# Performance work log

Measured on AMD Instinct MI355X. Metric: run time of the kernel, lower is better.

The kernel has to match this reference:

```python
import jax, jax.numpy as jnp
import numpy as np

TOP_K = 1024  # init top_k


def setup_inputs() -> dict:
    key = jax.random.key(0)
    ks = jax.random.split(key, 11)
    B, S, D, H = 8, 1024, 1024, 4096
    s = 0.02
    return {
        "inputs": jax.random.normal(ks[0], (B, S, D), jnp.float32),
        "up_w": jax.random.normal(ks[1], (H, D), jnp.float32) * s,
        "up_b": jax.random.normal(ks[2], (H,), jnp.float32) * s,
        "gate_w1": jax.random.normal(ks[3], (H, D), jnp.float32) * s,
        "gate_b1": jax.random.normal(ks[4], (H,), jnp.float32) * s,
        "gate_w2": jax.random.normal(ks[5], (H, H), jnp.float32) * s,
        "gate_b2": jax.random.normal(ks[6], (H,), jnp.float32) * s,
        "mod_w": jax.random.normal(ks[7], (H, D), jnp.float32) * s,
        "mod_b": jax.random.normal(ks[8], (H,), jnp.float32) * s,
        "down_w": jax.random.normal(ks[9], (D, H), jnp.float32) * s,
        "down_b": jax.random.normal(ks[10], (D,), jnp.float32) * s,
    }


def reference(inputs, up_w, up_b, gate_w1, gate_b1, gate_w2, gate_b2,
              mod_w, mod_b, down_w, down_b):
    B, S, D = inputs.shape
    H = up_w.shape[0]
    # gate: Linear -> ReLU -> Linear, scores [B,S,H]
    scores = jax.nn.relu(jnp.einsum('bsd,hd->bsh', inputs, gate_w1) + gate_b1)
    scores = jnp.einsum('bsh,gh->bsg', scores, gate_w2) + gate_b2
    flat_scores = scores.reshape(B, S * H)
    k = min(TOP_K * S, S * H)
    _, flat_idx = jax.lax.top_k(flat_scores, k)          # [B,k]
    hidden_idx = flat_idx % H                            # [B,k]
    # scatter writes mod.weight[h] at row h -> duplicates harmless -> boolean mask
    batch_idx = jnp.broadcast_to(jnp.arange(B)[:, None], (B, k))
    mask = jnp.zeros((B, H), bool).at[batch_idx, hidden_idx].set(True)
    # per-batch modified weights/bias (materialized like torch repeat+index_put)
    w = jnp.where(mask[:, :, None], mod_w[None], up_w[None])   # [B,H,D]
    b = jnp.where(mask, mod_b[None], up_b[None])               # [B,H]
    h = jnp.einsum('bsd,bhd->bsh', inputs, w) + b[:, None, :]
    h = jax.nn.silu(h)
    # dropout p=0.0 (eval) -> identity
    return jnp.einsum('bsh,dh->bsd', h, down_w) + down_b
```

## Files before the change

### kernel.cpp

```cpp
#include <hip/hip_runtime.h>
#include <cstdint>

typedef __attribute__((ext_vector_type(8))) short short8;
typedef __attribute__((ext_vector_type(4))) float floatx4;
typedef unsigned int uint32;

typedef const void __attribute__((address_space(1)))* gcptr;
typedef void __attribute__((address_space(3)))* lptr;

constexpr int Bn = 8, Sn = 1024, Dn = 1024, Hn = 4096;
constexpr uint32 KTOP = 1024u * 1024u;
constexpr uint32 SKBASE = 0xBB000000u;
constexpr uint32 EMAX = (1u << 27) - 1u;
constexpr uint32 WLO = 3645;
constexpr uint32 WHI = 4157;
constexpr uint32 CAP = 1u << 20;

constexpr size_t NX  = (size_t)Bn * Sn * Dn;
constexpr size_t NW1 = (size_t)Hn * Dn;
constexpr size_t NW2 = (size_t)Hn * Hn;
constexpr size_t NRS = (size_t)Bn * Sn * Hn;

constexpr size_t OFF_XH   = 0;
constexpr size_t OFF_XL   = OFF_XH  + 2 * NX;
constexpr size_t OFF_W1H  = OFF_XL  + 2 * NX;
constexpr size_t OFF_W1L  = OFF_W1H + 2 * NW1;
constexpr size_t OFF_W2H  = OFF_W1L + 2 * NW1;
constexpr size_t OFF_W2L  = OFF_W2H + 2 * NW2;
constexpr size_t OFF_RSH  = OFF_W2L + 2 * NW2;
constexpr size_t OFF_RSL  = OFF_RSH + 2 * NRS;
constexpr size_t OFF_HIST = OFF_RSL + 2 * NRS;
constexpr size_t OFF_HIST2= OFF_HIST + (size_t)Bn * 8192 * 4;
constexpr size_t OFF_HMAX = OFF_HIST2+ (size_t)Bn * 16384 * 4;
constexpr size_t OFF_META = OFF_HMAX + (size_t)Bn * Hn * 4;
constexpr size_t OFF_BSEL = OFF_META + 4096;
constexpr size_t OFF_MASK = OFF_BSEL + (size_t)Bn * Hn * 4;
constexpr size_t WS_SMALL = OFF_MASK + (size_t)Bn * Hn * 4;
constexpr size_t ZERO_BYTES = OFF_BSEL - OFF_HIST;
constexpr size_t OFF_BUF  = OFF_XL;

__device__ __forceinline__ ushort f2bf(float f) {
  uint32 u = __float_as_uint(f);
  u += 0x7fffu + ((u >> 16) & 1u);
  return (ushort)(u >> 16);
}
__device__ __forceinline__ float bf2f(ushort h) {
  return __uint_as_float(((uint32)h) << 16);
}
__device__ __forceinline__ uint32 skey(float v) {
  uint32 u = __float_as_uint(v);
  return (u & 0x80000000u) ? ~u : (u | 0x80000000u);
}
__device__ __forceinline__ uint32 ekey(uint32 key) {
  if (key <= SKBASE) return 0u;
  uint32 d = key - SKBASE;
  return d > EMAX ? EMAX : d;
}
__device__ __forceinline__ void g2l(const ushort* src, ushort* dst) {
  __builtin_amdgcn_global_load_lds((gcptr)src, (lptr)dst, 16, 0, 0);
}
__device__ __forceinline__ void stage_tile(ushort* lds, const ushort* gbase, int ldg, int tid) {
  const int w = tid >> 6;
  const int c0 = tid, c1 = tid + 256;
  g2l(gbase + (size_t)(c0 >> 2) * ldg + (c0 & 3) * 8, lds + (size_t)(w * 64) * 8);
  g2l(gbase + (size_t)(c1 >> 2) * ldg + (c1 & 3) * 8, lds + (size_t)(256 + w * 64) * 8);
}
__device__ __forceinline__ void stage_tile_sel(ushort* lds, const ushort* upw,
                                               const ushort* modw, const uint32* bm,
                                               int n0, int k0, int ldg, int tid) {
  const int w = tid >> 6;
  const int c0 = tid, c1 = tid + 256;
  const int r0 = n0 + (c0 >> 2), r1 = n0 + (c1 >> 2);
  const ushort* s0 = (bm[r0] ? modw : upw) + (size_t)r0 * ldg + k0 + (c0 & 3) * 8;
  const ushort* s1 = (bm[r1] ? modw : upw) + (size_t)r1 * ldg + k0 + (c1 & 3) * 8;
  g2l(s0, lds + (size_t)(w * 64) * 8);
  g2l(s1, lds + (size_t)(256 + w * 64) * 8);
}

__global__ __launch_bounds__(256) void cvt_split_k(const float4* __restrict__ x,
                                                   ushort* __restrict__ hi,
                                                   ushort* __restrict__ lo, int n4) {
  int stride = gridDim.x * 256;
  for (int i = blockIdx.x * 256 + threadIdx.x; i < n4; i += stride) {
    float4 v = x[i];
    ushort h0 = f2bf(v.x), h1 = f2bf(v.y), h2 = f2bf(v.z), h3 = f2bf(v.w);
    ushort4 hv; hv.x = h0; hv.y = h1; hv.z = h2; hv.w = h3;
    *(ushort4*)(hi + (size_t)i * 4) = hv;
    ushort4 lv;
    lv.x = f2bf(v.x - bf2f(h0)); lv.y = f2bf(v.y - bf2f(h1));
    lv.z = f2bf(v.z - bf2f(h2)); lv.w = f2bf(v.w - bf2f(h3));
    *(ushort4*)(lo + (size_t)i * 4) = lv;
  }
}
__global__ __launch_bounds__(256) void cvt_single_k(const float4* __restrict__ x,
                                                    ushort* __restrict__ hi, int n4) {
  int stride = gridDim.x * 256;
  for (int i = blockIdx.x * 256 + threadIdx.x; i < n4; i += stride) {
    float4 v = x[i];
    ushort4 hv; hv.x = f2bf(v.x); hv.y = f2bf(v.y); hv.z = f2bf(v.z); hv.w = f2bf(v.w);
    *(ushort4*)(hi + (size_t)i * 4) = hv;
  }
}
__global__ __launch_bounds__(256) void zero_out_k(float* __restrict__ o, int n) {
  int i = blockIdx.x * 256 + threadIdx.x;
  if (i < n) o[i] = 0.f;
}

constexpr int EPI_RELU = 0;
constexpr int EPI_SCORE = 1;
constexpr int EPI_SILU = 2;
constexpr int EPI_F32 = 3;

template <bool SPLIT, bool SELB, int EPI>
__global__ __launch_bounds__(256, SPLIT ? 3 : 2) void gemm_bt(
    const ushort* __restrict__ Ah, const ushort* __restrict__ Al,
    const ushort* __restrict__ Bh, const ushort* __restrict__ Bl,
    const uint32* __restrict__ bmask,
    int N, int K, long long a_bs, long long o_bs, long long bias_bs,
    const float* __restrict__ bias,
    void* __restrict__ outp, void* __restrict__ out2p,
    uint32* __restrict__ hist, uint32* __restrict__ hmax,
    uint32* __restrict__ buf, uint32* __restrict__ cnt) {
  __shared__ __align__(16) ushort lds[SPLIT ? 16384 : 8192];
  ushort* As = lds;
  ushort* Bs = lds + (SPLIT ? 8192 : 4096);

  const int tid = threadIdx.x;
  const int w = tid >> 6, l = tid & 63;
  const int wm = (w >> 1) << 6, wn = (w & 1) << 6;
  const int lm = l & 15, lq = l >> 4;
  const int m0 = blockIdx.y << 7, n0 = blockIdx.x << 7;
  const int z = blockIdx.z;

  const ushort* pAh = Ah + (size_t)z * a_bs + (size_t)m0 * K;
  const ushort* pAl = SPLIT ? Al + (size_t)z * a_bs + (size_t)m0 * K : nullptr;
  const ushort* pBh = SELB ? nullptr : Bh + (size_t)n0 * K;
  const ushort* pBl = (SPLIT && !SELB) ? Bl + (size_t)n0 * K : nullptr;
  const uint32* bm = SELB ? bmask + (size_t)z * Hn : nullptr;

  floatx4 acc[4][4];
#pragma unroll
  for (int i = 0; i < 4; i++)
#pragma unroll
    for (int j = 0; j < 4; j++) acc[i][j] = floatx4{0.f, 0.f, 0.f, 0.f};

  for (int k0 = 0; k0 < K; k0 += 32) {
    stage_tile(As, pAh + k0, K, tid);
    if constexpr (SELB)
      stage_tile_sel(Bs, Bh, Bl, bm, n0, k0, K, tid);
    else
      stage_tile(Bs, pBh + k0, K, tid);
    if constexpr (SPLIT) {
      stage_tile(As + 4096, pAl + k0, K, tid);
      stage_tile(Bs + 4096, pBl + k0, K, tid);
    }
    __syncthreads();
    short8 afh[4], bfh[4];
#pragma unroll
    for (int i = 0; i < 4; i++)
      afh[i] = *(const short8*)&As[(wm + i * 16 + lm) * 32 + lq * 8];
#pragma unroll
    for (int i = 0; i < 4; i++)
      bfh[i] = *(const short8*)&Bs[(wn + i * 16 + lm) * 32 + lq * 8];
#pragma unroll
    for (int mi = 0; mi < 4; mi++)
#pragma unroll
      for (int ni = 0; ni < 4; ni++)
        acc[mi][ni] = __builtin_amdgcn_mfma_f32_16x16x32_bf16(afh[mi], bfh[ni], acc[mi][ni], 0, 0, 0);
    if constexpr (SPLIT) {
      {
        short8 afl[4];
#pragma unroll
        for (int i = 0; i < 4; i++)
          afl[i] = *(const short8*)&As[4096 + (wm + i * 16 + lm) * 32 + lq * 8];
#pragma unroll
        for (int mi = 0; mi < 4; mi++)
#pragma unroll
          for (int ni = 0; ni < 4; ni++)
            acc[mi][ni] = __builtin_amdgcn_mfma_f32_16x16x32_bf16(afl[mi], bfh[ni], acc[mi][ni], 0, 0, 0);
      }
      {
        short8 bfl[4];
#pragma unroll
        for (int i = 0; i < 4; i++)
          bfl[i] = *(const short8*)&Bs[4096 + (wn + i * 16 + lm) * 32 + lq * 8];
#pragma unroll
        for (int mi = 0; mi < 4; mi++)
#pragma unroll
          for (int ni = 0; ni < 4; ni++)
            acc[mi][ni] = __builtin_amdgcn_mfma_f32_16x16x32_bf16(afh[mi], bfl[ni], acc[mi][ni], 0, 0, 0);
      }
    }
    __syncthreads();
  }

  if constexpr (EPI == EPI_SILU) {
    ushort* o = (ushort*)outp + (size_t)z * o_bs;
    const float* bb = bias + (size_t)z * bias_bs;
#pragma unroll
    for (int mi = 0; mi < 4; mi++)
#pragma unroll
      for (int ni = 0; ni < 4; ni++) {
        int gm = m0 + wm + mi * 16 + lq * 4;
        int gn = n0 + wn + ni * 16 + lm;
        float bnv = bb[gn];
#pragma unroll
        for (int r = 0; r < 4; r++) {
          float v = acc[mi][ni][r] + bnv;
          float s = v / (1.f + __expf(-v));
          o[(size_t)(gm + r) * N + gn] = f2bf(s);
        }
      }
  } else if constexpr (EPI == EPI_F32) {
    float* o = (float*)outp;
#pragma unroll
    for (int mi = 0; mi < 4; mi++)
#pragma unroll
      for (int ni = 0; ni < 4; ni++) {
        int gm = m0 + wm + mi * 16 + lq * 4;
        int gn = n0 + wn + ni * 16 + lm;
        float bnv = bias[gn];
#pragma unroll
        for (int r = 0; r < 4; r++)
          o[(size_t)(gm + r) * N + gn] = acc[mi][ni][r] + bnv;
      }
  }
}

#define LGKM0 do { asm volatile("s_waitcnt lgkmcnt(0)" ::: "memory"); \
                   __builtin_amdgcn_sched_barrier(0); } while (0)

__device__ __forceinline__ short8 fragld(const ushort* S, int r, int swz) {
  return *(const short8*)&S[r * 32 + swz];
}
__device__ __forceinline__ void stage256(ushort* d, const ushort* g,
                                         size_t soff0, size_t soff1, int dbase) {
  g2l(g + soff0, d + dbase);
  g2l(g + soff1, d + dbase + 4096);
}
__device__ __forceinline__ void mfma_block(floatx4 (&acc)[8][4], const short8 (&af)[4],
                                           int mi0, const short8 (&bf)[4]) {
#pragma unroll
  for (int mi = 0; mi < 4; mi++)
#pragma unroll
    for (int ni = 0; ni < 4; ni++)
      acc[mi0 + mi][ni] =
          __builtin_amdgcn_mfma_f32_16x16x32_bf16(af[mi], bf[ni], acc[mi0 + mi][ni], 0, 0, 0);
}

template <bool ST>
__device__ __forceinline__ void kstep256(
    floatx4 (&acc)[8][4], ushort (&lds)[2][4][8192], int p,
    const ushort* nA0, const ushort* nB0, const ushort* nA1, const ushort* nB1,
    size_t soff0, size_t soff1, int dbase, int swz, int lm, int wrow, int wcol) {
  const ushort* AhS = &lds[p][0][0];
  const ushort* BhS = &lds[p][1][0];
  const ushort* AlS = &lds[p][2][0];
  const ushort* BlS = &lds[p][3][0];
  ushort* dA0 = &lds[p ^ 1][0][0];
  ushort* dB0 = &lds[p ^ 1][1][0];
  ushort* dA1 = &lds[p ^ 1][2][0];
  ushort* dB1 = &lds[p ^ 1][3][0];

  short8 afh0[4], afh1[4], bfh[4];
#pragma unroll
  for (int i = 0; i < 4; i++) afh0[i] = fragld(AhS, wrow + i * 16 + lm, swz);
#pragma unroll
  for (int i = 0; i < 4; i++) bfh[i] = fragld(BhS, wcol + i * 16 + lm, swz);
  if constexpr (ST) stage256(dA0, nA0, soff0, soff1, dbase);
  __builtin_amdgcn_s_barrier();
  LGKM0;
  __builtin_amdgcn_s_setprio(1);
  mfma_block(acc, afh0, 0, bfh);
  __builtin_amdgcn_s_setprio(0);
  __builtin_amdgcn_s_barrier();
#pragma unroll
  for (int i = 0; i < 4; i++) afh1[i] = fragld(AhS, wrow + 64 + i * 16 + lm, swz);
  if constexpr (ST) stage256(dB0, nB0, soff0, soff1, dbase);
  __builtin_amdgcn_s_barrier();
  LGKM0;
  __builtin_amdgcn_s_setprio(1);
  mfma_block(acc, afh1, 4, bfh);
  __builtin_amdgcn_s_setprio(0);
  if constexpr (ST) asm volatile("s_waitcnt vmcnt(6)" ::: "memory");
  else              asm volatile("s_waitcnt vmcnt(2)" ::: "memory");
  __builtin_amdgcn_s_barrier();
  {
    short8 afl[4];
#pragma unroll
    for (int i = 0; i < 4; i++) afl[i] = fragld(AlS, wrow + i * 16 + lm, swz);
    if constexpr (ST) stage256(dA1, nA1, soff0, soff1, dbase);
    __builtin_amdgcn_s_barrier();
    LGKM0;
    __builtin_amdgcn_s_setprio(1);
    mfma_block(acc, afl, 0, bfh);
    __builtin_amdgcn_s_setprio(0);
    __builtin_amdgcn_s_barrier();
  }
  {
    short8 afl[4];
#pragma unroll
    for (int i = 0; i < 4; i++) afl[i] = fragld(AlS, wrow + 64 + i * 16 + lm, swz);
    if constexpr (ST) stage256(dB1, nB1, soff0, soff1, dbase);
    __builtin_amdgcn_s_barrier();
    LGKM0;
    __builtin_amdgcn_s_setprio(1);
    mfma_block(acc, afl, 4, bfh);
    __builtin_amdgcn_s_setprio(0);
    if constexpr (ST) asm volatile("s_waitcnt vmcnt(8)" ::: "memory");
    else              asm volatile("s_waitcnt vmcnt(0)" ::: "memory");
    __builtin_amdgcn_s_barrier();
  }
  {
    short8 bfl[4];
#pragma unroll
    for (int i = 0; i < 4; i++) bfl[i] = fragld(BlS, wcol + i * 16 + lm, swz);
    __builtin_amdgcn_s_barrier();
    LGKM0;
    __builtin_amdgcn_s_setprio(1);
    mfma_block(acc, afh0, 0, bfl);
    mfma_block(acc, afh1, 4, bfl);
    __builtin_amdgcn_s_setprio(0);
    if constexpr (ST) asm volatile("s_waitcnt vmcnt(4)" ::: "memory");
    __builtin_amdgcn_s_barrier();
  }
}

template <int EPI>
__global__ __launch_bounds__(512, 2) void gemm256(
    const ushort* __restrict__ Ah, const ushort* __restrict__ Al,
    const ushort* __restrict__ Bh, const ushort* __restrict__ Bl,
    int N, int K, const float* __restrict__ bias,
    ushort* __restrict__ outh, ushort* __restrict__ outl,
    uint32* __restrict__ hist, uint32* __restrict__ hmax,
    uint32* __restrict__ buf, uint32* __restrict__ cnt) {
  static_assert(EPI == EPI_RELU || EPI == EPI_SCORE, "gemm256 handles G1/G2 only");
  __shared__ __align__(16) ushort lds[2][4][8192];
  const int tid = threadIdx.x;
  const int l = tid & 63, w = tid >> 6;
  const int lm = l & 15, lq = l >> 4;
  const int swz = (lq ^ ((lm >> 1) & 3)) << 3;
  const int wrow = (w >> 2) << 7, wcol = (w & 3) << 6;
  const int m0 = blockIdx.y << 8, n0 = blockIdx.x << 8;

  const int cg = ((l & 3) ^ ((l >> 3) & 3)) << 3;
  const int r0 = (w << 4) + (l >> 2);
  const size_t soff0 = (size_t)r0 * K + cg;
  const size_t soff1 = soff0 + (size_t)128 * K;
  const int dbase = w << 9;

  const ushort* pA0 = Ah + (size_t)m0 * K;
  const ushort* pA1 = Al + (size_t)m0 * K;
  const ushort* pB0 = Bh + (size_t)n0 * K;
  const ushort* pB1 = Bl + (size_t)n0 * K;

  floatx4 acc[8][4];
#pragma unroll
  for (int i = 0; i < 8; i++)
#pragma unroll
    for (int j = 0; j < 4; j++) acc[i][j] = floatx4{0.f, 0.f, 0.f, 0.f};

  stage256(&lds[0][0][0], pA0, soff0, soff1, dbase);
  stage256(&lds[0][1][0], pB0, soff0, soff1, dbase);
  stage256(&lds[0][2][0], pA1, soff0, soff1, dbase);
  stage256(&lds[0][3][0], pB1, soff0, soff1, dbase);
  asm volatile("s_waitcnt vmcnt(4)" ::: "memory");
  __builtin_amdgcn_s_barrier();

  const int nk = K >> 5;
  int T = 0;
  for (; T < nk - 1; ++T) {
    const int ko = (T + 1) << 5;
    kstep256<true>(acc, lds, T & 1, pA0 + ko, pB0 + ko, pA1 + ko, pB1 + ko,
                   soff0, soff1, dbase, swz, lm, wrow, wcol);
  }
  kstep256<false>(acc, lds, T & 1, pA0, pB0, pA1, pB1,
                  soff0, soff1, dbase, swz, lm, wrow, wcol);

  if constexpr (EPI == EPI_RELU) {
#pragma unroll
    for (int mi = 0; mi < 8; mi++)
#pragma unroll
      for (int ni = 0; ni < 4; ni++) {
        const int gm = m0 + wrow + mi * 16 + lq * 4;
        const int gn = n0 + wcol + ni * 16 + lm;
        const float bnv = bias[gn];
#pragma unroll
        for (int r = 0; r < 4; r++) {
          float v = fmaxf(acc[mi][ni][r] + bnv, 0.f);
          ushort h = f2bf(v);
          size_t o = (size_t)(gm + r) * N + gn;
          outh[o] = h;
          outl[o] = f2bf(v - bf2f(h));
        }
      }
  } else {
    __syncthreads();
    uint32* hs = (uint32*)&lds[0][0][0];
    for (int i = tid; i < 8192; i += 512) hs[i] = 0;
    __syncthreads();
    const int batch = m0 >> 10;
    uint32 cntl = 0;
#pragma unroll
    for (int ni = 0; ni < 4; ni++) {
      const int gn = n0 + wcol + ni * 16 + lm;
      const float bnv = bias[gn];
      float vmax = -3.4e38f;
#pragma unroll
      for (int mi = 0; mi < 8; mi++) {
#pragma unroll
        for (int r = 0; r < 4; r++) {
          float v = acc[mi][ni][r] + bnv;
          uint32 e = ekey(skey(v));
          uint32 bk = e >> 14;
          atomicAdd(&hs[bk], 1u);
          if (bk >= WLO && bk <= WHI) cntl++;
          vmax = fmaxf(vmax, v);
        }
      }
      atomicMax(&hmax[batch * Hn + gn], skey(vmax));
    }
    __syncthreads();
    for (int i = tid; i < 8192; i += 512) {
      uint32 c = hs[i];
      if (c) atomicAdd(&hist[batch * 8192 + i], c);
    }
    __syncthreads();
    hs[tid] = cntl;
    __syncthreads();
    if (tid == 0) {
      uint32 run = 0;
      for (int i = 0; i < 512; i++) { uint32 t = hs[i]; hs[i] = run; run += t; }
      hs[512] = atomicAdd(&cnt[batch], run);
    }
    __syncthreads();
    uint32 off = hs[512] + hs[tid];
    uint32* bb = buf + (size_t)batch * CAP;
#pragma unroll
    for (int ni = 0; ni < 4; ni++) {
      const int gn = n0 + wcol + ni * 16 + lm;
      const float bnv = bias[gn];
#pragma unroll
      for (int mi = 0; mi < 8; mi++) {
#pragma unroll
        for (int r = 0; r < 4; r++) {
          float v = acc[mi][ni][r] + bnv;
          uint32 e = ekey(skey(v));
          uint32 bk = e >> 14;
          if (bk >= WLO && bk <= WHI) {
            if (off < CAP) bb[off] = e;
            off++;
          }
        }
      }
    }
  }
}

__global__ __launch_bounds__(256) void select1_k(const uint32* __restrict__ hist,
                                                 uint32* __restrict__ meta) {
  int b = blockIdx.x;
  const uint32* h = hist + b * 8192;
  __shared__ uint32 ps[256];
  uint32 s = 0;
  int base = threadIdx.x * 32;
  for (int i = 0; i < 32; i++) s += h[base + i];
  ps[threadIdx.x] = s;
  __syncthreads();
  if (threadIdx.x == 0) {
    uint32 cum = 0, need = 1;
    int j = 0;
    for (int c = 255; c >= 0; c--) {
      if (cum + ps[c] >= KTOP) {
        for (int i = c * 32 + 31;; i--) {
          uint32 hv = h[i];
          if (cum + hv >= KTOP) { j = i; need = KTOP - cum; break; }
          cum += hv;
        }
        break;
      }
      cum += ps[c];
    }
    meta[8 + b] = (uint32)j;
    meta[16 + b] = need;
    meta[b] = SKBASE + ((uint32)j << 14);
  }
}

__global__ __launch_bounds__(256) void refine_buf_k(const uint32* __restrict__ buf,
                                                    const uint32* __restrict__ meta,
                                                    uint32* __restrict__ hist2) {
  const uint32* cnt = meta + 32;
  size_t stride = (size_t)gridDim.x * 256;
  for (int b = 0; b < Bn; b++) {
    uint32 n = cnt[b] < CAP ? cnt[b] : CAP;
    uint32 j = meta[8 + b];
    const uint32* bb = buf + (size_t)b * CAP;
    for (size_t i = (size_t)blockIdx.x * 256 + threadIdx.x; i < n; i += stride) {
      uint32 e = bb[i];
      if ((e >> 14) == j) atomicAdd(&hist2[(size_t)b * 16384 + (e & 0x3FFFu)], 1u);
    }
  }
}

__global__ __launch_bounds__(256) void select2_k(const uint32* __restrict__ hist2,
                                                 uint32* __restrict__ meta) {
  int b = blockIdx.x;
  const uint32* h2 = hist2 + (size_t)b * 16384;
  __shared__ uint32 ps[256];
  uint32 s = 0;
  const uint32* p = h2 + (size_t)threadIdx.x * 64;
  for (int i = 0; i < 64; i += 4) {
    uint4 v = *(const uint4*)(p + i);
    s += v.x + v.y + v.z + v.w;
  }
  ps[threadIdx.x] = s;
  __syncthreads();
  if (threadIdx.x == 0) {
    uint32 j = meta[8 + b];
    uint32 valid = (j >= WLO && j <= WHI && meta[32 + b] <= CAP) ? 1u : 0u;
    if (valid) {
      uint32 need = meta[16 + b];
      uint32 cum = 0;
      int c = 255;
      for (; c > 0; c--) {
        if (cum + ps[c] >= need) break;
        cum += ps[c];
      }
      uint32 rem = 0;
      for (int i = 63; i >= 0; i--) {
        uint32 hv = h2[c * 64 + i];
        if (cum + hv >= need) { rem = (uint32)(c * 64 + i); break; }
        cum += hv;
      }
      meta[b] = SKBASE + (j << 14) + rem;
    }
  }
}

__global__ __launch_bounds__(256) void mask_k(const uint32* __restrict__ hmax,
                                              const uint32* __restrict__ meta,
                                              const float* __restrict__ modb,
                                              const float* __restrict__ upb,
                                              uint32* __restrict__ mask,
                                              float* __restrict__ bsel) {
  int i = blockIdx.x * 256 + threadIdx.x;
  int b = i >> 12, h = i & 4095;
  bool m = hmax[i] >= meta[b];
  mask[i] = m ? 1u : 0u;
  bsel[i] = m ? modb[h] : upb[h];
}

extern "C" void kernel_launch(void* const* d_in, const int* in_sizes, int n_in,
                              void* d_out, int out_size, void* d_ws, size_t ws_size,
                              hipStream_t stream) {
  (void)in_sizes; (void)n_in;
  const float* x    = (const float*)d_in[0];
  const float* up_w = (const float*)d_in[1];
  const float* up_b = (const float*)d_in[2];
  const float* g_w1 = (const float*)d_in[3];
  const float* g_b1 = (const float*)d_in[4];
  const float* g_w2 = (const float*)d_in[5];
  const float* g_b2 = (const float*)d_in[6];
  const float* mod_w= (const float*)d_in[7];
  const float* mod_b= (const float*)d_in[8];
  const float* dw   = (const float*)d_in[9];
  const float* db   = (const float*)d_in[10];
  float* out = (float*)d_out;

  if (ws_size < WS_SMALL) {
    zero_out_k<<<(out_size + 255) / 256, 256, 0, stream>>>(out, out_size);
    return;
  }

  char* ws = (char*)d_ws;
  ushort* XH  = (ushort*)(ws + OFF_XH);
  ushort* XL  = (ushort*)(ws + OFF_XL);
  ushort* W1H = (ushort*)(ws + OFF_W1H);
  ushort* W1L = (ushort*)(ws + OFF_W1L);
  ushort* W2H = (ushort*)(ws + OFF_W2H);
  ushort* W2L = (ushort*)(ws + OFF_W2L);
  ushort* RSH = (ushort*)(ws + OFF_RSH);
  ushort* RSL = (ushort*)(ws + OFF_RSL);
  uint32* HIST = (uint32*)(ws + OFF_HIST);
  uint32* HIST2= (uint32*)(ws + OFF_HIST2);
  uint32* HMAX = (uint32*)(ws + OFF_HMAX);
  uint32* META = (uint32*)(ws + OFF_META);
  float*  BSEL = (float*)(ws + OFF_BSEL);
  uint32* MASK = (uint32*)(ws + OFF_MASK);
  uint32* BUF  = (uint32*)(ws + OFF_BUF);
  ushort* UPW  = W1H;
  ushort* MODW = W1L;
  ushort* DWNW = XL;
  ushort* HBUF = RSH;

  hipMemsetAsync(ws + OFF_HIST, 0, ZERO_BYTES, stream);

  cvt_split_k<<<1024, 256, 0, stream>>>((const float4*)x, XH, XL, (int)(NX / 4));
  cvt_split_k<<<1024, 256, 0, stream>>>((const float4*)g_w1, W1H, W1L, (int)(NW1 / 4));
  cvt_split_k<<<2048, 256, 0, stream>>>((const float4*)g_w2, W2H, W2L, (int)(NW2 / 4));

  gemm256<EPI_RELU><<<dim3(Hn / 256, (Bn * Sn) / 256), 512, 0, stream>>>(
      XH, XL, W1H, W1L, Hn, Dn, g_b1, RSH, RSL, nullptr, nullptr, nullptr, nullptr);
  gemm256<EPI_SCORE><<<dim3(Hn / 256, (Bn * Sn) / 256), 512, 0, stream>>>(
      RSH, RSL, W2H, W2L, Hn, Hn, g_b2, nullptr, nullptr, HIST, HMAX, BUF, META + 32);

  select1_k<<<Bn, 256, 0, stream>>>(HIST, META);
  refine_buf_k<<<512, 256, 0, stream>>>(BUF, META, HIST2);
  select2_k<<<Bn, 256, 0, stream>>>(HIST2, META);
  mask_k<<<(Bn * Hn) / 256, 256, 0, stream>>>(HMAX, META, mod_b, up_b, MASK, BSEL);

  cvt_single_k<<<1024, 256, 0, stream>>>((const float4*)up_w, UPW, (int)(NW1 / 4));
  cvt_single_k<<<1024, 256, 0, stream>>>((const float4*)mod_w, MODW, (int)(NW1 / 4));
  cvt_single_k<<<1024, 256, 0, stream>>>((const float4*)dw, DWNW, (int)(NW1 / 4));

  gemm_bt<false, true, EPI_SILU><<<dim3(Hn / 128, Sn / 128, Bn), 256, 0, stream>>>(
      XH, nullptr, UPW, MODW, MASK, Hn, Dn,
      (long long)Sn * Dn, (long long)Sn * Hn, (long long)Hn,
      BSEL, HBUF, nullptr, nullptr, nullptr, nullptr, nullptr);
  gemm_bt<false, false, EPI_F32><<<dim3(Dn / 128, (Bn * Sn) / 128, 1), 256, 0, stream>>>(
      HBUF, nullptr, DWNW, nullptr, nullptr, Dn, Hn, 0, 0, 0, db, out, nullptr,
      nullptr, nullptr, nullptr, nullptr);
}
```

Baseline: 1.246 ms.

## Move SiLU up-projection to pipelined 256x256 gemm and reorder split-bf16 k-step

```diff
diff --git a/kernel.cpp b/kernel.cpp
--- a/kernel.cpp
+++ b/kernel.cpp
@@ -39,6 +39,8 @@
 constexpr size_t ZERO_BYTES = OFF_BSEL - OFF_HIST;
 constexpr size_t OFF_BUF  = OFF_XL;
 
+#define VMCNT(n) asm volatile("s_waitcnt vmcnt(" #n ")" ::: "memory")
+
 __device__ __forceinline__ ushort f2bf(float f) {
   uint32 u = __float_as_uint(f);
   u += 0x7fffu + ((u >> 16) & 1u);
@@ -64,17 +66,6 @@
   const int c0 = tid, c1 = tid + 256;
   g2l(gbase + (size_t)(c0 >> 2) * ldg + (c0 & 3) * 8, lds + (size_t)(w * 64) * 8);
   g2l(gbase + (size_t)(c1 >> 2) * ldg + (c1 & 3) * 8, lds + (size_t)(256 + w * 64) * 8);
-}
-__device__ __forceinline__ void stage_tile_sel(ushort* lds, const ushort* upw,
-                                               const ushort* modw, const uint32* bm,
-                                               int n0, int k0, int ldg, int tid) {
-  const int w = tid >> 6;
-  const int c0 = tid, c1 = tid + 256;
-  const int r0 = n0 + (c0 >> 2), r1 = n0 + (c1 >> 2);
-  const ushort* s0 = (bm[r0] ? modw : upw) + (size_t)r0 * ldg + k0 + (c0 & 3) * 8;
-  const ushort* s1 = (bm[r1] ? modw : upw) + (size_t)r1 * ldg + k0 + (c1 & 3) * 8;
-  g2l(s0, lds + (size_t)(w * 64) * 8);
-  g2l(s1, lds + (size_t)(256 + w * 64) * 8);
 }
 
 __global__ __launch_bounds__(256) void cvt_split_k(const float4* __restrict__ x,
@@ -118,9 +109,7 @@
     const uint32* __restrict__ bmask,
     int N, int K, long long a_bs, long long o_bs, long long bias_bs,
     const float* __restrict__ bias,
-    void* __restrict__ outp, void* __restrict__ out2p,
-    uint32* __restrict__ hist, uint32* __restrict__ hmax,
-    uint32* __restrict__ buf, uint32* __restrict__ cnt) {
+    void* __restrict__ outp, void* __restrict__ out2p) {
   __shared__ __align__(16) ushort lds[SPLIT ? 16384 : 8192];
   ushort* As = lds;
   ushort* Bs = lds + (SPLIT ? 8192 : 4096);
@@ -133,10 +122,7 @@
   const int z = blockIdx.z;
 
   const ushort* pAh = Ah + (size_t)z * a_bs + (size_t)m0 * K;
-  const ushort* pAl = SPLIT ? Al + (size_t)z * a_bs + (size_t)m0 * K : nullptr;
-  const ushort* pBh = SELB ? nullptr : Bh + (size_t)n0 * K;
-  const ushort* pBl = (SPLIT && !SELB) ? Bl + (size_t)n0 * K : nullptr;
-  const uint32* bm = SELB ? bmask + (size_t)z * Hn : nullptr;
+  const ushort* pBh = Bh + (size_t)n0 * K;
 
   floatx4 acc[4][4];
 #pragma unroll
@@ -146,14 +132,7 @@
 
   for (int k0 = 0; k0 < K; k0 += 32) {
     stage_tile(As, pAh + k0, K, tid);
-    if constexpr (SELB)
-      stage_tile_sel(Bs, Bh, Bl, bm, n0, k0, K, tid);
-    else
-      stage_tile(Bs, pBh + k0, K, tid);
-    if constexpr (SPLIT) {
-      stage_tile(As + 4096, pAl + k0, K, tid);
-      stage_tile(Bs + 4096, pBl + k0, K, tid);
-    }
+    stage_tile(Bs, pBh + k0, K, tid);
     __syncthreads();
     short8 afh[4], bfh[4];
 #pragma unroll
@@ -167,30 +146,6 @@
 #pragma unroll
       for (int ni = 0; ni < 4; ni++)
         acc[mi][ni] = __builtin_amdgcn_mfma_f32_16x16x32_bf16(afh[mi], bfh[ni], acc[mi][ni], 0, 0, 0);
-    if constexpr (SPLIT) {
-      {
-        short8 afl[4];
-#pragma unroll
-        for (int i = 0; i < 4; i++)
-          afl[i] = *(const short8*)&As[4096 + (wm + i * 16 + lm) * 32 + lq * 8];
-#pragma unroll
-        for (int mi = 0; mi < 4; mi++)
-#pragma unroll
-          for (int ni = 0; ni < 4; ni++)
-            acc[mi][ni] = __builtin_amdgcn_mfma_f32_16x16x32_bf16(afl[mi], bfh[ni], acc[mi][ni], 0, 0, 0);
-      }
-      {
-        short8 bfl[4];
-#pragma unroll
-        for (int i = 0; i < 4; i++)
-          bfl[i] = *(const short8*)&Bs[4096 + (wn + i * 16 + lm) * 32 + lq * 8];
-#pragma unroll
-        for (int mi = 0; mi < 4; mi++)
-#pragma unroll
-          for (int ni = 0; ni < 4; ni++)
-            acc[mi][ni] = __builtin_amdgcn_mfma_f32_16x16x32_bf16(afh[mi], bfl[ni], acc[mi][ni], 0, 0, 0);
-      }
-    }
     __syncthreads();
   }
 
@@ -227,16 +182,8 @@
   }
 }
 
-#define LGKM0 do { asm volatile("s_waitcnt lgkmcnt(0)" ::: "memory"); \
-                   __builtin_amdgcn_sched_barrier(0); } while (0)
-
 __device__ __forceinline__ short8 fragld(const ushort* S, int r, int swz) {
   return *(const short8*)&S[r * 32 + swz];
-}
-__device__ __forceinline__ void stage256(ushort* d, const ushort* g,
-                                         size_t soff0, size_t soff1, int dbase) {
-  g2l(g + soff0, d + dbase);
-  g2l(g + soff1, d + dbase + 4096);
 }
 __device__ __forceinline__ void mfma_block(floatx4 (&acc)[8][4], const short8 (&af)[4],
                                            int mi0, const short8 (&bf)[4]) {
@@ -249,99 +196,127 @@
 }
 
 template <bool ST>
-__device__ __forceinline__ void kstep256(
-    floatx4 (&acc)[8][4], ushort (&lds)[2][4][8192], int p,
-    const ushort* nA0, const ushort* nB0, const ushort* nA1, const ushort* nB1,
-    size_t soff0, size_t soff1, int dbase, int swz, int lm, int wrow, int wcol) {
-  const ushort* AhS = &lds[p][0][0];
-  const ushort* BhS = &lds[p][1][0];
-  const ushort* AlS = &lds[p][2][0];
-  const ushort* BlS = &lds[p][3][0];
-  ushort* dA0 = &lds[p ^ 1][0][0];
-  ushort* dB0 = &lds[p ^ 1][1][0];
-  ushort* dA1 = &lds[p ^ 1][2][0];
-  ushort* dB1 = &lds[p ^ 1][3][0];
-
-  short8 afh0[4], afh1[4], bfh[4];
-#pragma unroll
-  for (int i = 0; i < 4; i++) afh0[i] = fragld(AhS, wrow + i * 16 + lm, swz);
-#pragma unroll
-  for (int i = 0; i < 4; i++) bfh[i] = fragld(BhS, wcol + i * 16 + lm, swz);
-  if constexpr (ST) stage256(dA0, nA0, soff0, soff1, dbase);
-  __builtin_amdgcn_s_barrier();
-  LGKM0;
-  __builtin_amdgcn_s_setprio(1);
-  mfma_block(acc, afh0, 0, bfh);
-  __builtin_amdgcn_s_setprio(0);
-  __builtin_amdgcn_s_barrier();
-#pragma unroll
-  for (int i = 0; i < 4; i++) afh1[i] = fragld(AhS, wrow + 64 + i * 16 + lm, swz);
-  if constexpr (ST) stage256(dB0, nB0, soff0, soff1, dbase);
-  __builtin_amdgcn_s_barrier();
-  LGKM0;
-  __builtin_amdgcn_s_setprio(1);
-  mfma_block(acc, afh1, 4, bfh);
-  __builtin_amdgcn_s_setprio(0);
-  if constexpr (ST) asm volatile("s_waitcnt vmcnt(6)" ::: "memory");
-  else              asm volatile("s_waitcnt vmcnt(2)" ::: "memory");
-  __builtin_amdgcn_s_barrier();
-  {
-    short8 afl[4];
-#pragma unroll
-    for (int i = 0; i < 4; i++) afl[i] = fragld(AlS, wrow + i * 16 + lm, swz);
-    if constexpr (ST) stage256(dA1, nA1, soff0, soff1, dbase);
-    __builtin_amdgcn_s_barrier();
-    LGKM0;
-    __builtin_amdgcn_s_setprio(1);
-    mfma_block(acc, afl, 0, bfh);
-    __builtin_amdgcn_s_setprio(0);
-    __builtin_amdgcn_s_barrier();
-  }
-  {
-    short8 afl[4];
-#pragma unroll
-    for (int i = 0; i < 4; i++) afl[i] = fragld(AlS, wrow + 64 + i * 16 + lm, swz);
-    if constexpr (ST) stage256(dB1, nB1, soff0, soff1, dbase);
-    __builtin_amdgcn_s_barrier();
-    LGKM0;
-    __builtin_amdgcn_s_setprio(1);
-    mfma_block(acc, afl, 4, bfh);
-    __builtin_amdgcn_s_setprio(0);
-    if constexpr (ST) asm volatile("s_waitcnt vmcnt(8)" ::: "memory");
-    else              asm volatile("s_waitcnt vmcnt(0)" ::: "memory");
-    __builtin_amdgcn_s_barrier();
-  }
-  {
-    short8 bfl[4];
-#pragma unroll
-    for (int i = 0; i < 4; i++) bfl[i] = fragld(BlS, wcol + i * 16 + lm, swz);
-    __builtin_amdgcn_s_barrier();
-    LGKM0;
-    __builtin_amdgcn_s_setprio(1);
-    mfma_block(acc, afh0, 0, bfl);
-    mfma_block(acc, afh1, 4, bfl);
-    __builtin_amdgcn_s_setprio(0);
-    if constexpr (ST) asm volatile("s_waitcnt vmcnt(4)" ::: "memory");
-    __builtin_amdgcn_s_barrier();
-  }
-}
-
-template <int EPI>
+__device__ __forceinline__ void kstep_sp(
+    floatx4 (&acc)[8][4], ushort* ldsb, int p, int ko,
+    const ushort* sAh0, const ushort* sAh1, const ushort* sBh0, const ushort* sBh1,
+    const ushort* sAl0, const ushort* sAl1, const ushort* sBl0, const ushort* sBl1,
+    int dbase, int swz, int lm, int wrow, int wcol) {
+  const ushort* AhS = ldsb + (p * 4 + 0) * 8192;
+  const ushort* BhS = ldsb + (p * 4 + 1) * 8192;
+  const ushort* AlS = ldsb + (p * 4 + 2) * 8192;
+  const ushort* BlS = ldsb + (p * 4 + 3) * 8192;
+  ushort* dAh = ldsb + ((p ^ 1) * 4 + 0) * 8192;
+  ushort* dBh = ldsb + ((p ^ 1) * 4 + 1) * 8192;
+  ushort* dAl = ldsb + ((p ^ 1) * 4 + 2) * 8192;
+  ushort* dBl = ldsb + ((p ^ 1) * 4 + 3) * 8192;
+
+  short8 ahT[4], ahB[4], bh[4], bl[4];
+#pragma unroll
+  for (int i = 0; i < 4; i++) ahT[i] = fragld(AhS, wrow + i * 16 + lm, swz);
+#pragma unroll
+  for (int i = 0; i < 4; i++) bh[i]  = fragld(BhS, wcol + i * 16 + lm, swz);
+#pragma unroll
+  for (int i = 0; i < 4; i++) ahB[i] = fragld(AhS, wrow + 64 + i * 16 + lm, swz);
+  if constexpr (ST) { g2l(sAh0 + ko, dAh + dbase); g2l(sAh1 + ko, dAh + dbase + 4096); }
+  __builtin_amdgcn_s_barrier();
+  __builtin_amdgcn_s_setprio(1);
+  mfma_block(acc, ahT, 0, bh);
+  __builtin_amdgcn_s_setprio(0);
+  if constexpr (ST) VMCNT(2); else VMCNT(0);
+  __builtin_amdgcn_s_barrier();
+#pragma unroll
+  for (int i = 0; i < 4; i++) bl[i] = fragld(BlS, wcol + i * 16 + lm, swz);
+  if constexpr (ST) { g2l(sBh0 + ko, dBh + dbase); g2l(sBh1 + ko, dBh + dbase + 4096); }
+  __builtin_amdgcn_s_barrier();
+  __builtin_amdgcn_s_setprio(1);
+  mfma_block(acc, ahB, 4, bh);
+  __builtin_amdgcn_s_setprio(0);
+  __builtin_amdgcn_s_barrier();
+  if constexpr (ST) { g2l(sAl0 + ko, dAl + dbase); g2l(sAl1 + ko, dAl + dbase + 4096); }
+  __builtin_amdgcn_s_barrier();
+  __builtin_amdgcn_s_setprio(1);
+  mfma_block(acc, ahT, 0, bl);
+  __builtin_amdgcn_s_setprio(0);
+  __builtin_amdgcn_s_barrier();
+  short8 alT[4];
+#pragma unroll
+  for (int i = 0; i < 4; i++) alT[i] = fragld(AlS, wrow + i * 16 + lm, swz);
+  if constexpr (ST) { g2l(sBl0 + ko, dBl + dbase); g2l(sBl1 + ko, dBl + dbase + 4096); }
+  __builtin_amdgcn_s_barrier();
+  __builtin_amdgcn_s_setprio(1);
+  mfma_block(acc, ahB, 4, bl);
+  __builtin_amdgcn_s_setprio(0);
+  __builtin_amdgcn_s_barrier();
+  short8 alB[4];
+#pragma unroll
+  for (int i = 0; i < 4; i++) alB[i] = fragld(AlS, wrow + 64 + i * 16 + lm, swz);
+  __builtin_amdgcn_s_barrier();
+  __builtin_amdgcn_s_setprio(1);
+  mfma_block(acc, alT, 0, bh);
+  __builtin_amdgcn_s_setprio(0);
+  __builtin_amdgcn_s_barrier();
+  __builtin_amdgcn_s_setprio(1);
+  mfma_block(acc, alB, 4, bh);
+  __builtin_amdgcn_s_setprio(0);
+  if constexpr (ST) VMCNT(4);
+  __builtin_amdgcn_s_barrier();
+}
+
+template <bool ST>
+__device__ __forceinline__ void kstep_ns(
+    floatx4 (&acc)[8][4], ushort* ldsb, int p, int ko,
+    const ushort* sA0, const ushort* sA1, const ushort* sB0, const ushort* sB1,
+    int dbase, int swz, int lm, int wrow, int wcol) {
+  const ushort* AS = ldsb + (p * 2 + 0) * 8192;
+  const ushort* BS = ldsb + (p * 2 + 1) * 8192;
+  ushort* dA = ldsb + ((p ^ 1) * 2 + 0) * 8192;
+  ushort* dB = ldsb + ((p ^ 1) * 2 + 1) * 8192;
+  short8 aT[4], aB[4], b[4];
+#pragma unroll
+  for (int i = 0; i < 4; i++) aT[i] = fragld(AS, wrow + i * 16 + lm, swz);
+#pragma unroll
+  for (int i = 0; i < 4; i++) b[i]  = fragld(BS, wcol + i * 16 + lm, swz);
+#pragma unroll
+  for (int i = 0; i < 4; i++) aB[i] = fragld(AS, wrow + 64 + i * 16 + lm, swz);
+  if constexpr (ST) {
+    g2l(sA0 + ko, dA + dbase); g2l(sA1 + ko, dA + dbase + 4096);
+    g2l(sB0 + ko, dB + dbase); g2l(sB1 + ko, dB + dbase + 4096);
+  }
+  __builtin_amdgcn_s_barrier();
+  __builtin_amdgcn_s_setprio(1);
+  mfma_block(acc, aT, 0, b);
+  __builtin_amdgcn_s_setprio(0);
+  __builtin_amdgcn_s_barrier();
+  __builtin_amdgcn_s_setprio(1);
+  mfma_block(acc, aB, 4, b);
+  __builtin_amdgcn_s_setprio(0);
+  if constexpr (ST) VMCNT(0);
+  __builtin_amdgcn_s_barrier();
+}
+
+template <int EPI, bool SPLIT, bool SELB>
 __global__ __launch_bounds__(512, 2) void gemm256(
     const ushort* __restrict__ Ah, const ushort* __restrict__ Al,
     const ushort* __restrict__ Bh, const ushort* __restrict__ Bl,
-    int N, int K, const float* __restrict__ bias,
+    const uint32* __restrict__ bmask,
+    int N, int K, long long a_bs, long long o_bs, long long bias_bs,
+    const float* __restrict__ bias,
     ushort* __restrict__ outh, ushort* __restrict__ outl,
     uint32* __restrict__ hist, uint32* __restrict__ hmax,
     uint32* __restrict__ buf, uint32* __restrict__ cnt) {
-  static_assert(EPI == EPI_RELU || EPI == EPI_SCORE, "gemm256 handles G1/G2 only");
-  __shared__ __align__(16) ushort lds[2][4][8192];
+  static_assert(EPI != EPI_SCORE || SPLIT, "score path is split");
+  static_assert(!(SPLIT && SELB), "unused combo");
+  constexpr int NSUB = SPLIT ? 4 : 2;
+  __shared__ __align__(16) ushort lds[2 * NSUB * 8192];
+  ushort* ldsb = &lds[0];
+
   const int tid = threadIdx.x;
   const int l = tid & 63, w = tid >> 6;
   const int lm = l & 15, lq = l >> 4;
   const int swz = (lq ^ ((lm >> 1) & 3)) << 3;
   const int wrow = (w >> 2) << 7, wcol = (w & 3) << 6;
   const int m0 = blockIdx.y << 8, n0 = blockIdx.x << 8;
+  const int z = blockIdx.z;
 
   const int cg = ((l & 3) ^ ((l >> 3) & 3)) << 3;
   const int r0 = (w << 4) + (l >> 2);
@@ -349,10 +324,33 @@
   const size_t soff1 = soff0 + (size_t)128 * K;
   const int dbase = w << 9;
 
-  const ushort* pA0 = Ah + (size_t)m0 * K;
-  const ushort* pA1 = Al + (size_t)m0 * K;
-  const ushort* pB0 = Bh + (size_t)n0 * K;
-  const ushort* pB1 = Bl + (size_t)n0 * K;
+  const ushort* pA = Ah + (size_t)z * a_bs + (size_t)m0 * K;
+  const ushort* sAh0 = pA + soff0;
+  const ushort* sAh1 = pA + soff1;
+  const ushort* sAl0 = nullptr;
+  const ushort* sAl1 = nullptr;
+  if constexpr (SPLIT) {
+    const ushort* pAl = Al + (size_t)z * a_bs + (size_t)m0 * K;
+    sAl0 = pAl + soff0;
+    sAl1 = pAl + soff1;
+  }
+  const ushort* sBh0;
+  const ushort* sBh1;
+  if constexpr (SELB) {
+    const uint32* bm = bmask + (size_t)z * Hn;
+    const int gr0 = n0 + r0, gr1 = gr0 + 128;
+    sBh0 = (bm[gr0] ? Bl : Bh) + (size_t)gr0 * K + cg;
+    sBh1 = (bm[gr1] ? Bl : Bh) + (size_t)gr1 * K + cg;
+  } else {
+    sBh0 = Bh + (size_t)n0 * K + soff0;
+    sBh1 = Bh + (size_t)n0 * K + soff1;
+  }
+  const ushort* sBl0 = nullptr;
+  const ushort* sBl1 = nullptr;
+  if constexpr (SPLIT) {
+    sBl0 = Bl + (size_t)n0 * K + soff0;
+    sBl1 = Bl + (size_t)n0 * K + soff1;
+  }
 
   floatx4 acc[8][4];
 #pragma unroll
@@ -360,22 +358,34 @@
 #pragma unroll
     for (int j = 0; j < 4; j++) acc[i][j] = floatx4{0.f, 0.f, 0.f, 0.f};
 
-  stage256(&lds[0][0][0], pA0, soff0, soff1, dbase);
-  stage256(&lds[0][1][0], pB0, soff0, soff1, dbase);
-  stage256(&lds[0][2][0], pA1, soff0, soff1, dbase);
-  stage256(&lds[0][3][0], pB1, soff0, soff1, dbase);
-  asm volatile("s_waitcnt vmcnt(4)" ::: "memory");
+  g2l(sAh0, ldsb + 0 * 8192 + dbase); g2l(sAh1, ldsb + 0 * 8192 + dbase + 4096);
+  g2l(sBh0, ldsb + 1 * 8192 + dbase); g2l(sBh1, ldsb + 1 * 8192 + dbase + 4096);
+  if constexpr (SPLIT) {
+    g2l(sAl0, ldsb + 2 * 8192 + dbase); g2l(sAl1, ldsb + 2 * 8192 + dbase + 4096);
+    g2l(sBl0, ldsb + 3 * 8192 + dbase); g2l(sBl1, ldsb + 3 * 8192 + dbase + 4096);
+    VMCNT(4);
+  } else {
+    VMCNT(0);
+  }
   __builtin_amdgcn_s_barrier();
 
   const int nk = K >> 5;
   int T = 0;
   for (; T < nk - 1; ++T) {
     const int ko = (T + 1) << 5;
-    kstep256<true>(acc, lds, T & 1, pA0 + ko, pB0 + ko, pA1 + ko, pB1 + ko,
-                   soff0, soff1, dbase, swz, lm, wrow, wcol);
-  }
-  kstep256<false>(acc, lds, T & 1, pA0, pB0, pA1, pB1,
-                  soff0, soff1, dbase, swz, lm, wrow, wcol);
+    if constexpr (SPLIT)
+      kstep_sp<true>(acc, ldsb, T & 1, ko, sAh0, sAh1, sBh0, sBh1, sAl0, sAl1, sBl0, sBl1,
+                     dbase, swz, lm, wrow, wcol);
+    else
+      kstep_ns<true>(acc, ldsb, T & 1, ko, sAh0, sAh1, sBh0, sBh1,
+                     dbase, swz, lm, wrow, wcol);
+  }
+  if constexpr (SPLIT)
+    kstep_sp<false>(acc, ldsb, T & 1, 0, sAh0, sAh1, sBh0, sBh1, sAl0, sAl1, sBl0, sBl1,
+                    dbase, swz, lm, wrow, wcol);
+  else
+    kstep_ns<false>(acc, ldsb, T & 1, 0, sAh0, sAh1, sBh0, sBh1,
+                    dbase, swz, lm, wrow, wcol);
 
   if constexpr (EPI == EPI_RELU) {
 #pragma unroll
@@ -394,9 +404,26 @@
           outl[o] = f2bf(v - bf2f(h));
         }
       }
-  } else {
-    __syncthreads();
-    uint32* hs = (uint32*)&lds[0][0][0];
+  } else if constexpr (EPI == EPI_SILU) {
+    ushort* o = outh + (size_t)z * o_bs;
+    const float* bb = bias + (size_t)z * bias_bs;
+#pragma unroll
+    for (int mi = 0; mi < 8; mi++)
+#pragma unroll
+      for (int ni = 0; ni < 4; ni++) {
+        const int gm = m0 + wrow + mi * 16 + lq * 4;
+        const int gn = n0 + wcol + ni * 16 + lm;
+        const float bnv = bb[gn];
+#pragma unroll
+        for (int r = 0; r < 4; r++) {
+          float v = acc[mi][ni][r] + bnv;
+          float s = v / (1.f + __expf(-v));
+          o[(size_t)(gm + r) * N + gn] = f2bf(s);
+        }
+      }
+  } else if constexpr (EPI == EPI_SCORE) {
+    __syncthreads();
+    uint32* hs = (uint32*)ldsb;
     for (int i = tid; i < 8192; i += 512) hs[i] = 0;
     __syncthreads();
     const int batch = m0 >> 10;
@@ -600,10 +627,12 @@
   cvt_split_k<<<1024, 256, 0, stream>>>((const float4*)g_w1, W1H, W1L, (int)(NW1 / 4));
   cvt_split_k<<<2048, 256, 0, stream>>>((const float4*)g_w2, W2H, W2L, (int)(NW2 / 4));
 
-  gemm256<EPI_RELU><<<dim3(Hn / 256, (Bn * Sn) / 256), 512, 0, stream>>>(
-      XH, XL, W1H, W1L, Hn, Dn, g_b1, RSH, RSL, nullptr, nullptr, nullptr, nullptr);
-  gemm256<EPI_SCORE><<<dim3(Hn / 256, (Bn * Sn) / 256), 512, 0, stream>>>(
-      RSH, RSL, W2H, W2L, Hn, Hn, g_b2, nullptr, nullptr, HIST, HMAX, BUF, META + 32);
+  gemm256<EPI_RELU, true, false><<<dim3(Hn / 256, (Bn * Sn) / 256), 512, 0, stream>>>(
+      XH, XL, W1H, W1L, nullptr, Hn, Dn, 0, 0, 0, g_b1, RSH, RSL,
+      nullptr, nullptr, nullptr, nullptr);
+  gemm256<EPI_SCORE, true, false><<<dim3(Hn / 256, (Bn * Sn) / 256), 512, 0, stream>>>(
+      RSH, RSL, W2H, W2L, nullptr, Hn, Hn, 0, 0, 0, g_b2, nullptr, nullptr,
+      HIST, HMAX, BUF, META + 32);
 
   select1_k<<<Bn, 256, 0, stream>>>(HIST, META);
   refine_buf_k<<<512, 256, 0, stream>>>(BUF, META, HIST2);
@@ -614,11 +643,10 @@
   cvt_single_k<<<1024, 256, 0, stream>>>((const float4*)mod_w, MODW, (int)(NW1 / 4));
   cvt_single_k<<<1024, 256, 0, stream>>>((const float4*)dw, DWNW, (int)(NW1 / 4));
 
-  gemm_bt<false, true, EPI_SILU><<<dim3(Hn / 128, Sn / 128, Bn), 256, 0, stream>>>(
+  gemm256<EPI_SILU, false, true><<<dim3(Hn / 256, Sn / 256, Bn), 512, 0, stream>>>(
       XH, nullptr, UPW, MODW, MASK, Hn, Dn,
       (long long)Sn * Dn, (long long)Sn * Hn, (long long)Hn,
       BSEL, HBUF, nullptr, nullptr, nullptr, nullptr, nullptr);
   gemm_bt<false, false, EPI_F32><<<dim3(Dn / 128, (Bn * Sn) / 128, 1), 256, 0, stream>>>(
-      HBUF, nullptr, DWNW, nullptr, nullptr, Dn, Hn, 0, 0, 0, db, out, nullptr,
-      nullptr, nullptr, nullptr, nullptr);
-}
+      HBUF, nullptr, DWNW, nullptr, nullptr, Dn, Hn, 0, 0, 0, db, out, nullptr);
+}
```

New measurement: 1.256 ms. Within noise of the previous version (+0.8%).
